# Performance work log

Measured on AMD Instinct MI355X. Metric: run time of the kernel, lower is better.

Reference implementation:

```python
import jax, jax.numpy as jnp
import numpy as np

Q_LEN, KV_LEN, N_HEADS, HEAD_DIM = 2048, 4096, 16, 64
NEG_INF = -1e9


def _causal_prefix_mask(q_len, kv_len):
    # query i (global position prefix+i) may attend to keys j <= prefix + i
    prefix = kv_len - q_len
    i = jnp.arange(q_len)[:, None]
    j = jnp.arange(kv_len)[None, :]
    allowed = j <= (prefix + i)
    return jnp.where(allowed, 0.0, NEG_INF).astype(jnp.float32)[None, None]  # [1,1,q,kv]


def setup_inputs() -> dict:
    key = jax.random.key(0)
    kq, kk, kv = jax.random.split(key, 3)
    query = jax.random.normal(kq, (1, N_HEADS, Q_LEN, HEAD_DIM), dtype=jnp.float32)
    k = jax.random.normal(kk, (1, N_HEADS, KV_LEN, HEAD_DIM), dtype=jnp.float32)
    v = jax.random.normal(kv, (1, N_HEADS, KV_LEN, HEAD_DIM), dtype=jnp.float32)
    attn_mask = _causal_prefix_mask(Q_LEN, KV_LEN)
    return {"query": query, "key": k, "value": v, "attn_mask": attn_mask}


def reference(query, key, value, attn_mask):
    # Equivalent math of SlicedFusedSDPA.forward: chunked causal SDPA with
    # online-softmax merge == one full masked softmax attention.
    # scale=None -> 1/sqrt(head_dim); dropout_p=0; is_causal=True encoded in attn_mask.
    scale = 1.0 / np.sqrt(query.shape[-1]).astype(np.float32)
    scores = jnp.einsum('bhqd,bhkd->bhqk', query, key) * scale + attn_mask  # [B,H,Q,KV]
    probs = jax.nn.softmax(scores, axis=-1)
    out = jnp.einsum('bhqk,bhkd->bhqd', probs, value)
    return out.astype(query.dtype)
```

## Files before the change

### kernel.cpp

```cpp
#include <hip/hip_runtime.h>
#include <hip/hip_bf16.h>

#define NH 16
#define QL 2048
#define KVL 4096
#define DH 64
#define PREFIX (KVL - QL)
#define NT 64
#define TUS 8192
#define PSTR32 34
#define SCALE 0.18033688011112043f

typedef __attribute__((ext_vector_type(8))) _Float16 f16x8;
typedef __attribute__((ext_vector_type(2))) _Float16 f16x2;
typedef __attribute__((ext_vector_type(8))) short short8;
typedef __attribute__((ext_vector_type(4))) float f32x4;
typedef __attribute__((ext_vector_type(16))) float f32x16;
typedef unsigned int u32;

static __device__ __forceinline__ float exp2_fast(float x) {
    float r; asm("v_exp_f32 %0, %1" : "=v"(r) : "v"(x)); return r;
}
static __device__ __forceinline__ u32 pkrtz(float lo, float hi) {
    u32 r; asm("v_cvt_pkrtz_f16_f32 %0, %1, %2" : "=v"(r) : "v"(lo), "v"(hi)); return r;
}
static __device__ __forceinline__ void plswap(u32& x, u32& y) {
    asm("v_permlane32_swap_b32 %0, %1" : "+v"(x), "+v"(y));
}
#define MFMAH(a, b, c) __builtin_amdgcn_mfma_f32_32x32x16_f16(a, b, c, 0, 0, 0)

static __device__ __forceinline__ void gload_lds16(const ushort* g, ushort* l) {
    __builtin_amdgcn_global_load_lds(
        (const __attribute__((address_space(1))) u32*)g,
        (__attribute__((address_space(3))) u32*)l, 16, 0, 0);
}

static __device__ __forceinline__ ushort f2bf(float x) {
    union { float f; u32 u; } v; v.f = x;
    u32 r = v.u + 0x7fffu + ((v.u >> 16) & 1u);
    return (ushort)(r >> 16);
}
static __device__ __forceinline__ float bf2f(ushort h) {
    union { u32 u; float f; } v; v.u = ((u32)h) << 16;
    return v.f;
}

__global__ void convKV(const float* __restrict__ K, const float* __restrict__ V,
                       ushort* __restrict__ ws) {
    const int half = blockIdx.x >> 11;
    const int gid  = (blockIdx.x & 2047) * 256 + threadIdx.x;
    const int lane = gid & 63;
    const int fidx = (gid >> 6) & 7;
    const int tile = (gid >> 9) & 63;
    const int h    = gid >> 15;
    const int lq = lane & 31, hi = lane >> 5;
    f16x8 o;
    if (half == 0) {
        const int t = fidx >> 2, ks = fidx & 3;
        const int kv = tile * 64 + t * 32 + lq;
        const float* src = K + ((size_t)h * KVL + kv) * DH + ks * 16 + hi * 8;
        const float4 a = *(const float4*)src;
        const float4 b = *(const float4*)(src + 4);
        const float v[8] = {a.x, a.y, a.z, a.w, b.x, b.y, b.z, b.w};
        #pragma unroll
        for (int j = 0; j < 8; ++j) o[j] = (_Float16)v[j];
        *(f16x8*)(ws + (size_t)(h * NT + tile) * TUS + fidx * 512 + lane * 8) = o;
    } else {
        const int dt = fidx >> 2, ks = fidx & 3;
        const int d  = dt * 32 + lq;
        const float* src = V + ((size_t)h * KVL + tile * 64 + ks * 16 + hi * 8) * DH + d;
        #pragma unroll
        for (int j = 0; j < 8; ++j) o[j] = (_Float16)src[j * DH];
        *(f16x8*)(ws + (size_t)(h * NT + tile) * TUS + 4096 + fidx * 512 + lane * 8) = o;
    }
}

template<int NSPLIT>
__global__ __launch_bounds__(256, 4)
void sdpa_main(const float* __restrict__ Q, const ushort* __restrict__ ws,
               float* __restrict__ part)
{
    __shared__ ushort lds[4][2][2048];

    const int tid  = threadIdx.x;
    const int lane = tid & 63;
    const int w    = tid >> 6;
    const int lq   = lane & 31;
    const int hi   = lane >> 5;

    const int bid = blockIdx.x;
    const int xcd = bid & 7;
    const int k   = bid >> 3;
    int h, qwA, sp;
    if constexpr (NSPLIT == 4) {
        const int hsub = k & 1;
        const int kk   = k >> 1;
        h   = xcd * 2 + hsub;
        qwA = kk >> 1;
        sp  = (w >> 1) * 2 + (kk & 1);
    } else {
        h   = xcd * 2 + (k & 1);
        qwA = k >> 1;
        sp  = w >> 1;
    }
    const int qw = (w & 1) ? (63 - qwA) : qwA;
    const int qb = qw * 32;

    const int ntt = (PREFIX + qb + 32) >> 5;
    const int t0  = (ntt * sp) / NSPLIT;
    const int t1  = (ntt * (sp + 1)) / NSPLIT;

    f16x8 qh[4];
    {
        const float* qp = Q + ((size_t)h * QL + qb + lq) * DH + hi * 8;
        #pragma unroll
        for (int ks = 0; ks < 4; ++ks) {
            const float4 a = *(const float4*)(qp + ks * 16);
            const float4 b = *(const float4*)(qp + ks * 16 + 4);
            const float vv[8] = {a.x, a.y, a.z, a.w, b.x, b.y, b.z, b.w};
            #pragma unroll
            for (int jj = 0; jj < 8; ++jj)
                qh[ks][jj] = (_Float16)(vv[jj] * SCALE);
        }
    }

    f32x16 oacc[2];
    #pragma unroll
    for (int dt = 0; dt < 2; ++dt)
        #pragma unroll
        for (int r = 0; r < 16; ++r) oacc[dt][r] = 0.f;
    float m = 0.0f, lsum = 0.f;

    const ushort* hb = ws + (size_t)h * NT * TUS + lane * 8;

    #define KSRC(IT) (hb + (size_t)((IT) >> 1) * TUS + ((IT) & 1) * 2048)
    #define KSTAGE(IT, B) do {                                             \
        const ushort* _s = KSRC(IT);                                       \
        ushort* _d = &lds[w][(B)][0];                                      \
        gload_lds16(_s,        _d);                                        \
        gload_lds16(_s + 512,  _d + 512);                                  \
        gload_lds16(_s + 1024, _d + 1024);                                 \
        gload_lds16(_s + 1536, _d + 1536);                                 \
    } while (0)

    KSTAGE(t0, t0 & 1);
    if (t0 + 1 < t1) KSTAGE(t0 + 1, (t0 + 1) & 1);

    for (int it = t0; it < t1; ++it) {
        asm volatile("s_waitcnt vmcnt(4)" ::: "memory");
        __builtin_amdgcn_sched_barrier(0);

        const ushort* bV = hb + (size_t)(it >> 1) * TUS + 4096 + (it & 1) * 1024;
        f16x8 vf[4];
        vf[0] = *(const f16x8*)(bV);
        vf[1] = *(const f16x8*)(bV + 512);
        vf[2] = *(const f16x8*)(bV + 2048);
        vf[3] = *(const f16x8*)(bV + 2560);

        const ushort* kb = &lds[w][it & 1][lane * 8];
        f16x8 kf0 = *(const f16x8*)(kb);
        f16x8 kf1 = *(const f16x8*)(kb + 512);
        f16x8 kf2 = *(const f16x8*)(kb + 1024);
        f16x8 kf3 = *(const f16x8*)(kb + 1536);

        f32x16 sT;
        #pragma unroll
        for (int r = 0; r < 16; ++r) sT[r] = 0.f;
        __builtin_amdgcn_s_setprio(1);
        sT = MFMAH(kf0, qh[0], sT);
        sT = MFMAH(kf1, qh[1], sT);
        sT = MFMAH(kf2, qh[2], sT);
        sT = MFMAH(kf3, qh[3], sT);
        __builtin_amdgcn_s_setprio(0);

        if (it + 2 < t1) KSTAGE(it + 2, it & 1);

        const int kv0 = it * 32;
        if (kv0 + 32 > PREFIX + qb) {
            const int kvlim = PREFIX + qb + lq - kv0;
            #pragma unroll
            for (int r = 0; r < 16; ++r) {
                const int c = (r & 3) + 8 * (r >> 2) + 4 * hi;
                if (c > kvlim) sT[r] = -1e30f;
            }
        }

        float tmx[8];
        #pragma unroll
        for (int i = 0; i < 8; ++i) tmx[i] = fmaxf(sT[i], sT[i + 8]);
        #pragma unroll
        for (int ss = 4; ss > 0; ss >>= 1)
            #pragma unroll
            for (int i = 0; i < ss; ++i) tmx[i] = fmaxf(tmx[i], tmx[i + ss]);
        float mx = fmaxf(tmx[0], __shfl_xor(tmx[0], 32));
        if (__any(mx > m + 8.0f)) {
            const float mn  = fmaxf(m, mx);
            const float fsc = exp2_fast(m - mn);
            lsum *= fsc;
            #pragma unroll
            for (int dt = 0; dt < 2; ++dt)
                #pragma unroll
                for (int r = 0; r < 16; ++r) oacc[dt][r] *= fsc;
            m = mn;
        }
        #pragma unroll
        for (int r = 0; r < 16; ++r) sT[r] = exp2_fast(sT[r] - m);
        float ts[8];
        #pragma unroll
        for (int i = 0; i < 8; ++i) ts[i] = sT[i] + sT[i + 8];
        #pragma unroll
        for (int ss = 4; ss > 0; ss >>= 1)
            #pragma unroll
            for (int i = 0; i < ss; ++i) ts[i] += ts[i + ss];
        lsum += ts[0];

        u32 x0 = pkrtz(sT[0],  sT[1]);
        u32 x1 = pkrtz(sT[2],  sT[3]);
        u32 y0 = pkrtz(sT[4],  sT[5]);
        u32 y1 = pkrtz(sT[6],  sT[7]);
        u32 x2 = pkrtz(sT[8],  sT[9]);
        u32 x3 = pkrtz(sT[10], sT[11]);
        u32 y2 = pkrtz(sT[12], sT[13]);
        u32 y3 = pkrtz(sT[14], sT[15]);
        plswap(x0, y0); plswap(x1, y1);
        plswap(x2, y2); plswap(x3, y3);
        union { u32 u[4]; f16x8 v; } p0, p1;
        p0.u[0] = x0; p0.u[1] = x1; p0.u[2] = y0; p0.u[3] = y1;
        p1.u[0] = x2; p1.u[1] = x3; p1.u[2] = y2; p1.u[3] = y3;

        __builtin_amdgcn_s_setprio(1);
        oacc[0] = MFMAH(vf[0], p0.v, oacc[0]);
        oacc[0] = MFMAH(vf[1], p1.v, oacc[0]);
        oacc[1] = MFMAH(vf[2], p0.v, oacc[1]);
        oacc[1] = MFMAH(vf[3], p1.v, oacc[1]);
        __builtin_amdgcn_s_setprio(0);
    }
    #undef KSTAGE
    #undef KSRC

    const float ltot = lsum + __shfl_xor(lsum, 32);
    const float linv = 1.0f / ltot;
    u32* pr = (u32*)part + ((size_t)(sp * NH + h) * QL + qb + lq) * PSTR32;
    #pragma unroll
    for (int dt = 0; dt < 2; ++dt)
        #pragma unroll
        for (int a = 0; a < 4; ++a) {
            const u32 w0 = pkrtz(oacc[dt][a * 4 + 0] * linv, oacc[dt][a * 4 + 1] * linv);
            const u32 w1 = pkrtz(oacc[dt][a * 4 + 2] * linv, oacc[dt][a * 4 + 3] * linv);
            pr[dt * 16 + a * 4 + hi * 2 + 0] = w0;
            pr[dt * 16 + a * 4 + hi * 2 + 1] = w1;
        }
    if (hi == 0) pr[32] = __float_as_uint(m + log2f(ltot));
}

template<int N>
__global__ void combineH(const u32* __restrict__ part, float* __restrict__ O) {
    const int r = blockIdx.x * 8 + (threadIdx.x >> 5);
    const int p = threadIdx.x & 31;
    float g[N], M = -1e30f;
    #pragma unroll
    for (int j = 0; j < N; ++j) {
        g[j] = __uint_as_float(part[((size_t)j * NH * QL + r) * PSTR32 + 32]);
        M = fmaxf(M, g[j]);
    }
    float a0 = 0.f, a1 = 0.f, wsum = 0.f;
    #pragma unroll
    for (int j = 0; j < N; ++j) {
        const float wj = exp2f(g[j] - M);
        union { u32 u; f16x2 h; } v;
        v.u = part[((size_t)j * NH * QL + r) * PSTR32 + p];
        a0 += wj * (float)v.h[0];
        a1 += wj * (float)v.h[1];
        wsum += wj;
    }
    const float inv = 1.0f / wsum;
    float* op = O + (size_t)r * DH + p * 2;
    op[0] = a0 * inv;
    op[1] = a1 * inv;
}

#define QT 64
#define KBf 32
#define KSTR 72
#define VSTR 40
#define PSTR 40
#define SCALE_E 0.125f

__global__ __launch_bounds__(256, 2)
void sdpa_fallback(const float* __restrict__ Q, const float* __restrict__ K,
                   const float* __restrict__ V, float* __restrict__ O)
{
    __shared__ ushort sKh[KBf][KSTR];
    __shared__ ushort sKl[KBf][KSTR];
    __shared__ ushort sVt[DH][VSTR];
    __shared__ ushort sPf[4][16][PSTR];

    const int tid  = threadIdx.x;
    const int lane = tid & 63;
    const int w    = tid >> 6;
    const int h    = blockIdx.y;
    const int q0   = blockIdx.x * QT;
    const int qb   = q0 + w * 16;
    const int lrow = lane & 15;
    const int lgrp = lane >> 4;

    short8 qh[2], ql[2];
    {
        const float* qp = Q + ((size_t)h * QL + (qb + lrow)) * DH;
        #pragma unroll
        for (int dh = 0; dh < 2; ++dh) {
            const int d0 = dh * 32 + lgrp * 8;
            #pragma unroll
            for (int jj = 0; jj < 8; ++jj) {
                float x = qp[d0 + jj] * SCALE_E;
                ushort hb = f2bf(x);
                qh[dh][jj] = (short)hb;
                ql[dh][jj] = (short)f2bf(x - bf2f(hb));
            }
        }
    }

    f32x4 oacc[4];
    float m_r[4], l_r[4];
    #pragma unroll
    for (int n = 0; n < 4; ++n) { oacc[n][0]=0.f; oacc[n][1]=0.f; oacc[n][2]=0.f; oacc[n][3]=0.f; }
    #pragma unroll
    for (int r = 0; r < 4; ++r) { m_r[r] = -1e30f; l_r[r] = 0.f; }

    const int nkv = min(KVL, PREFIX + q0 + QT);

    for (int kv0 = 0; kv0 < nkv; kv0 += KBf) {
        __syncthreads();
        {
            const int r  = tid >> 3;
            const int d0 = (tid & 7) * 8;
            const float* kp = K + ((size_t)h * KVL + (kv0 + r)) * DH + d0;
            const float* vp = V + ((size_t)h * KVL + (kv0 + r)) * DH + d0;
            short8 vh, vl;
            #pragma unroll
            for (int jj = 0; jj < 8; ++jj) {
                float x = kp[jj];
                ushort hb = f2bf(x);
                vh[jj] = (short)hb;
                vl[jj] = (short)f2bf(x - bf2f(hb));
            }
            *(short8*)&sKh[r][d0] = vh;
            *(short8*)&sKl[r][d0] = vl;
            #pragma unroll
            for (int jj = 0; jj < 8; ++jj)
                sVt[d0 + jj][r] = f2bf(vp[jj]);
        }
        __syncthreads();

        f32x4 s[2];
        #pragma unroll
        for (int t = 0; t < 2; ++t) { s[t][0]=0.f; s[t][1]=0.f; s[t][2]=0.f; s[t][3]=0.f; }
        #pragma unroll
        for (int t = 0; t < 2; ++t) {
            #pragma unroll
            for (int dh = 0; dh < 2; ++dh) {
                const short8 kh = *(const short8*)&sKh[t*16 + lrow][dh*32 + lgrp*8];
                const short8 kl = *(const short8*)&sKl[t*16 + lrow][dh*32 + lgrp*8];
                s[t] = __builtin_amdgcn_mfma_f32_16x16x32_bf16(qh[dh], kh, s[t], 0, 0, 0);
                s[t] = __builtin_amdgcn_mfma_f32_16x16x32_bf16(qh[dh], kl, s[t], 0, 0, 0);
                s[t] = __builtin_amdgcn_mfma_f32_16x16x32_bf16(ql[dh], kh, s[t], 0, 0, 0);
            }
        }

        if (kv0 + KBf > PREFIX + qb) {
            #pragma unroll
            for (int t = 0; t < 2; ++t)
                #pragma unroll
                for (int r = 0; r < 4; ++r) {
                    const int kv = kv0 + t*16 + lrow;
                    const int q  = qb + lgrp*4 + r;
                    if (kv > PREFIX + q) s[t][r] = -1e30f;
                }
        }

        float tmax[4];
        #pragma unroll
        for (int r = 0; r < 4; ++r) tmax[r] = fmaxf(s[0][r], s[1][r]);
        #pragma unroll
        for (int off = 1; off <= 8; off <<= 1)
            #pragma unroll
            for (int r = 0; r < 4; ++r) tmax[r] = fmaxf(tmax[r], __shfl_xor(tmax[r], off, 64));

        float f[4];
        #pragma unroll
        for (int r = 0; r < 4; ++r) {
            const float mn = fmaxf(m_r[r], tmax[r]);
            f[r] = __expf(m_r[r] - mn);
            m_r[r] = mn;
        }
        #pragma unroll
        for (int t = 0; t < 2; ++t)
            #pragma unroll
            for (int r = 0; r < 4; ++r) s[t][r] = __expf(s[t][r] - m_r[r]);

        float rs[4];
        #pragma unroll
        for (int r = 0; r < 4; ++r) rs[r] = s[0][r] + s[1][r];
        #pragma unroll
        for (int off = 1; off <= 8; off <<= 1)
            #pragma unroll
            for (int r = 0; r < 4; ++r) rs[r] += __shfl_xor(rs[r], off, 64);
        #pragma unroll
        for (int r = 0; r < 4; ++r) l_r[r] = l_r[r] * f[r] + rs[r];
        #pragma unroll
        for (int n = 0; n < 4; ++n)
            #pragma unroll
            for (int r = 0; r < 4; ++r) oacc[n][r] *= f[r];

        #pragma unroll
        for (int t = 0; t < 2; ++t)
            #pragma unroll
            for (int r = 0; r < 4; ++r)
                sPf[w][lgrp*4 + r][t*16 + lrow] = f2bf(s[t][r]);
        asm volatile("s_waitcnt lgkmcnt(0)" ::: "memory");
        __builtin_amdgcn_sched_barrier(0);

        const short8 pa = *(const short8*)&sPf[w][lrow][lgrp*8];
        #pragma unroll
        for (int n = 0; n < 4; ++n) {
            const short8 vb = *(const short8*)&sVt[n*16 + lrow][lgrp*8];
            oacc[n] = __builtin_amdgcn_mfma_f32_16x16x32_bf16(pa, vb, oacc[n], 0, 0, 0);
        }
    }

    float inv[4];
    #pragma unroll
    for (int r = 0; r < 4; ++r) inv[r] = 1.0f / l_r[r];
    float* op = O + ((size_t)h * QL + qb) * DH;
    #pragma unroll
    for (int n = 0; n < 4; ++n)
        #pragma unroll
        for (int r = 0; r < 4; ++r)
            op[(lgrp*4 + r) * DH + n*16 + lrow] = oacc[n][r] * inv[r];
}

extern "C" void kernel_launch(void* const* d_in, const int* in_sizes, int n_in,
                              void* d_out, int out_size, void* d_ws, size_t ws_size,
                              hipStream_t stream) {
    const float* Q = (const float*)d_in[0];
    const float* K = (const float*)d_in[1];
    const float* V = (const float*)d_in[2];
    float* O = (float*)d_out;
    const size_t KVWS  = (size_t)NH * NT * TUS * 2;
    const size_t PARTH = (size_t)NH * QL * PSTR32 * 4;
    ushort* wsKV = (ushort*)d_ws;
    float*  part = (float*)((char*)d_ws + KVWS);

    if (ws_size >= KVWS + 4 * PARTH) {
        hipLaunchKernelGGL(convKV, dim3(4096), dim3(256), 0, stream, K, V, wsKV);
        hipLaunchKernelGGL(sdpa_main<4>, dim3(1024), dim3(256), 0, stream, Q, wsKV, part);
        hipLaunchKernelGGL(combineH<4>, dim3(4096), dim3(256), 0, stream, (const u32*)part, O);
    } else if (ws_size >= KVWS + 2 * PARTH) {
        hipLaunchKernelGGL(convKV, dim3(4096), dim3(256), 0, stream, K, V, wsKV);
        hipLaunchKernelGGL(sdpa_main<2>, dim3(512), dim3(256), 0, stream, Q, wsKV, part);
        hipLaunchKernelGGL(combineH<2>, dim3(4096), dim3(256), 0, stream, (const u32*)part, O);
    } else {
        hipLaunchKernelGGL(sdpa_fallback, dim3(32, 16), dim3(256), 0, stream, Q, K, V, O);
    }
}
```

Before: 68.13 us.

## Drop LDS K staging and regroup NSPLIT=4 work so block waves share KV range

```diff
diff --git a/kernel.cpp b/kernel.cpp
--- a/kernel.cpp
+++ b/kernel.cpp
@@ -28,12 +28,6 @@
     asm("v_permlane32_swap_b32 %0, %1" : "+v"(x), "+v"(y));
 }
 #define MFMAH(a, b, c) __builtin_amdgcn_mfma_f32_32x32x16_f16(a, b, c, 0, 0, 0)
-
-static __device__ __forceinline__ void gload_lds16(const ushort* g, ushort* l) {
-    __builtin_amdgcn_global_load_lds(
-        (const __attribute__((address_space(1))) u32*)g,
-        (__attribute__((address_space(3))) u32*)l, 16, 0, 0);
-}
 
 static __device__ __forceinline__ ushort f2bf(float x) {
     union { float f; u32 u; } v; v.f = x;
@@ -80,8 +74,6 @@
 void sdpa_main(const float* __restrict__ Q, const ushort* __restrict__ ws,
                float* __restrict__ part)
 {
-    __shared__ ushort lds[4][2][2048];
-
     const int tid  = threadIdx.x;
     const int lane = tid & 63;
     const int w    = tid >> 6;
@@ -91,24 +83,25 @@
     const int bid = blockIdx.x;
     const int xcd = bid & 7;
     const int k   = bid >> 3;
-    int h, qwA, sp;
+    int h, qb, sp, ntt;
     if constexpr (NSPLIT == 4) {
         const int hsub = k & 1;
         const int kk   = k >> 1;
         h   = xcd * 2 + hsub;
-        qwA = kk >> 1;
-        sp  = (w >> 1) * 2 + (kk & 1);
+        const int qB = kk >> 2;
+        sp  = kk & 3;
+        qb  = qB * 128 + w * 32;
+        ntt = (PREFIX + qB * 128 + 128) >> 5;
     } else {
         h   = xcd * 2 + (k & 1);
-        qwA = k >> 1;
+        const int qwA = k >> 1;
         sp  = w >> 1;
-    }
-    const int qw = (w & 1) ? (63 - qwA) : qwA;
-    const int qb = qw * 32;
-
-    const int ntt = (PREFIX + qb + 32) >> 5;
-    const int t0  = (ntt * sp) / NSPLIT;
-    const int t1  = (ntt * (sp + 1)) / NSPLIT;
+        const int qw = (w & 1) ? (63 - qwA) : qwA;
+        qb  = qw * 32;
+        ntt = (PREFIX + qb + 32) >> 5;
+    }
+    const int t0 = (ntt * sp) / NSPLIT;
+    const int t1 = (ntt * (sp + 1)) / NSPLIT;
 
     f16x8 qh[4];
     {
@@ -133,47 +126,29 @@
 
     const ushort* hb = ws + (size_t)h * NT * TUS + lane * 8;
 
-    #define KSRC(IT) (hb + (size_t)((IT) >> 1) * TUS + ((IT) & 1) * 2048)
-    #define KSTAGE(IT, B) do {                                             \
-        const ushort* _s = KSRC(IT);                                       \
-        ushort* _d = &lds[w][(B)][0];                                      \
-        gload_lds16(_s,        _d);                                        \
-        gload_lds16(_s + 512,  _d + 512);                                  \
-        gload_lds16(_s + 1024, _d + 1024);                                 \
-        gload_lds16(_s + 1536, _d + 1536);                                 \
-    } while (0)
-
-    KSTAGE(t0, t0 & 1);
-    if (t0 + 1 < t1) KSTAGE(t0 + 1, (t0 + 1) & 1);
-
     for (int it = t0; it < t1; ++it) {
-        asm volatile("s_waitcnt vmcnt(4)" ::: "memory");
-        __builtin_amdgcn_sched_barrier(0);
-
-        const ushort* bV = hb + (size_t)(it >> 1) * TUS + 4096 + (it & 1) * 1024;
-        f16x8 vf[4];
+        const int s = it & 1;
+        const ushort* b64 = hb + (size_t)(it >> 1) * TUS;
+        const ushort* bK  = b64 + s * 2048;
+        const ushort* bV  = b64 + 4096 + s * 1024;
+
+        f16x8 kf[4], vf[4];
+        #pragma unroll
+        for (int f = 0; f < 4; ++f) kf[f] = *(const f16x8*)(bK + f * 512);
         vf[0] = *(const f16x8*)(bV);
         vf[1] = *(const f16x8*)(bV + 512);
         vf[2] = *(const f16x8*)(bV + 2048);
         vf[3] = *(const f16x8*)(bV + 2560);
 
-        const ushort* kb = &lds[w][it & 1][lane * 8];
-        f16x8 kf0 = *(const f16x8*)(kb);
-        f16x8 kf1 = *(const f16x8*)(kb + 512);
-        f16x8 kf2 = *(const f16x8*)(kb + 1024);
-        f16x8 kf3 = *(const f16x8*)(kb + 1536);
-
         f32x16 sT;
         #pragma unroll
         for (int r = 0; r < 16; ++r) sT[r] = 0.f;
         __builtin_amdgcn_s_setprio(1);
-        sT = MFMAH(kf0, qh[0], sT);
-        sT = MFMAH(kf1, qh[1], sT);
-        sT = MFMAH(kf2, qh[2], sT);
-        sT = MFMAH(kf3, qh[3], sT);
+        sT = MFMAH(kf[0], qh[0], sT);
+        sT = MFMAH(kf[1], qh[1], sT);
+        sT = MFMAH(kf[2], qh[2], sT);
+        sT = MFMAH(kf[3], qh[3], sT);
         __builtin_amdgcn_s_setprio(0);
-
-        if (it + 2 < t1) KSTAGE(it + 2, it & 1);
 
         const int kv0 = it * 32;
         if (kv0 + 32 > PREFIX + qb) {
@@ -235,8 +210,6 @@
         oacc[1] = MFMAH(vf[3], p1.v, oacc[1]);
         __builtin_amdgcn_s_setprio(0);
     }
-    #undef KSTAGE
-    #undef KSRC
 
     const float ltot = lsum + __shfl_xor(lsum, 32);
     const float linv = 1.0f / ltot;
```

Result: faster. 64.83 us (-4.8%).
